# Kernel optimization log

Measured on AMD Instinct MI355X. Metric: run time of the kernel, lower is better.

The kernel has to match this reference:

```python
import jax, jax.numpy as jnp
import numpy as np

MAX_DISP = 4          # displacement radius -> 9x9 = 81 output channels
B, C, H, W = 8, 128, 96, 160


def setup_inputs() -> dict:
    key = jax.random.key(0)
    k1, k2 = jax.random.split(key)
    tensorFirst = jax.random.normal(k1, (B, C, H, W), dtype=jnp.float32)
    tensorSecond = jax.random.normal(k2, (B, C, H, W), dtype=jnp.float32)
    return {"tensorFirst": tensorFirst, "tensorSecond": tensorSecond}


def correlation(first, second):
    # first, second: [B, C, H, W]
    b, c, h, w = first.shape
    d = MAX_DISP
    pad = jnp.pad(second, ((0, 0), (0, 0), (d, d), (d, d)))  # [B,C,H+8,W+8]
    inv_c = jnp.asarray(1.0 / c, dtype=first.dtype)
    # channel order: (dy+4)*9 + (dx+4), dx fastest (matches CUDA kernel)
    chans = [
        (first * pad[:, :, dy:dy + h, dx:dx + w]).sum(axis=1) * inv_c
        for dy in range(2 * d + 1)
        for dx in range(2 * d + 1)
    ]
    return jnp.stack(chans, axis=1)  # [B, 81, H, W]


def reference(tensorFirst, tensorSecond):
    return correlation(tensorFirst, tensorSecond)
```

## Files before the change

kernel.cpp:

```cpp
#include <hip/hip_runtime.h>
#include <stdint.h>


typedef __attribute__((ext_vector_type(8))) short bf16x8;
typedef __attribute__((ext_vector_type(4))) float f32x4;

constexpr int Bn = 8, Cn = 128, Hn = 96, Wn = 160;
constexpr int CHS = Hn * Wn;

__device__ __forceinline__ uint32_t bf16rne(float f) {
    uint32_t u = __float_as_uint(f);
    return (u + 0x7FFFu + ((u >> 16) & 1u)) >> 16;
}
__device__ __forceinline__ uint32_t pk(float a, float b) {
    return bf16rne(a) | (bf16rne(b) << 16);
}

__global__ __launch_bounds__(512, 4)
void corrfused(const float* __restrict__ first, const float* __restrict__ second,
               float* __restrict__ out)
{
    __shared__ uint4 smem[16 * 32 * 4];

    const int tid  = threadIdx.x;
    const int w    = tid >> 6;
    const int lane = tid & 63;
    const int quad = lane >> 4;
    const int n16  = lane & 15;
    const int r    = w;

    const int d    = (int)blockIdx.x + 10 * ((int)blockIdx.y + 12 * (int)blockIdx.z);
    const int tile = (d & 7) * 120 + (d >> 3);
    const int b    = tile / 120;
    const int rem  = tile % 120;
    const int y0   = (rem / 10) * 8;
    const int x0   = (rem % 10) * 16;
    const int y    = y0 + r;

    const float* sb = second + (size_t)b * Cn * CHS;
    int goff[4], lpos[4];
    bool val[4];
    #pragma unroll
    for (int i = 0; i < 4; ++i) {
        int e   = tid + i * 512;
        int row = e >> 7;
        int xw  = (e >> 2) & 31;
        int q   = e & 3;
        int gy  = y0 + row - 4, gx = x0 + xw - 8;
        val[i]  = (gy >= 0) && (gy < Hn) && (gx >= 0) && (gx < Wn);
        goff[i] = val[i] ? (8 * q * CHS + gy * Wn + gx) : 0;
        lpos[i] = (row * 32 + xw) * 4 + ((q + xw + (xw >> 2)) & 3);
    }

    int bo[2];
    #pragma unroll
    for (int t = 0; t < 2; ++t) {
        int xwr = 16 * t + n16;
        bo[t] = xwr * 4 + ((quad + xwr + (xwr >> 2)) & 3);
    }

    const float* fp = first + (size_t)b * Cn * CHS + (size_t)y * Wn + x0 + n16;

    f32x4 acc[9][2];
    #pragma unroll
    for (int dy = 0; dy < 9; ++dy)
        #pragma unroll
        for (int t = 0; t < 2; ++t)
            acc[dy][t] = (f32x4){0.f, 0.f, 0.f, 0.f};

    float f0[2][8];
    #pragma unroll
    for (int i = 0; i < 2; ++i)
        #pragma unroll
        for (int j = 0; j < 8; ++j)
            f0[i][j] = sb[goff[i] + (size_t)j * CHS];

    #pragma unroll
    for (int kc = 0; kc < 4; ++kc) {
        #pragma unroll
        for (int i = 0; i < 2; ++i) {
            uint4 o;
            o.x = pk(f0[i][0], f0[i][1]); o.y = pk(f0[i][2], f0[i][3]);
            o.z = pk(f0[i][4], f0[i][5]); o.w = pk(f0[i][6], f0[i][7]);
            if (!val[i]) o = make_uint4(0u, 0u, 0u, 0u);
            smem[lpos[i]] = o;
        }
        float f1[2][8], fa[8];
        #pragma unroll
        for (int i = 0; i < 2; ++i)
            #pragma unroll
            for (int j = 0; j < 8; ++j)
                f1[i][j] = sb[goff[2 + i] + (size_t)(32 * kc + j) * CHS];
        #pragma unroll
        for (int j = 0; j < 8; ++j)
            fa[j] = fp[(size_t)(32 * kc + 8 * quad + j) * CHS];
        #pragma unroll
        for (int i = 0; i < 2; ++i) {
            uint4 o;
            o.x = pk(f1[i][0], f1[i][1]); o.y = pk(f1[i][2], f1[i][3]);
            o.z = pk(f1[i][4], f1[i][5]); o.w = pk(f1[i][6], f1[i][7]);
            if (!val[2 + i]) o = make_uint4(0u, 0u, 0u, 0u);
            smem[lpos[2 + i]] = o;
        }
        bf16x8 aF;
        {
            union { uint32_t u[4]; bf16x8 v; } cv;
            cv.u[0] = pk(fa[0], fa[1]); cv.u[1] = pk(fa[2], fa[3]);
            cv.u[2] = pk(fa[4], fa[5]); cv.u[3] = pk(fa[6], fa[7]);
            aF = cv.v;
        }
        __syncthreads();
        if (kc < 3) {
            #pragma unroll
            for (int i = 0; i < 2; ++i)
                #pragma unroll
                for (int j = 0; j < 8; ++j)
                    f0[i][j] = sb[goff[i] + (size_t)(32 * (kc + 1) + j) * CHS];
        }
        #pragma unroll
        for (int dy = 0; dy < 9; ++dy) {
            const int rb = (r + dy) * 128;
            #pragma unroll
            for (int t = 0; t < 2; ++t) {
                union { uint4 u; bf16x8 v; } bf;
                bf.u = smem[rb + bo[t]];
                acc[dy][t] = __builtin_amdgcn_mfma_f32_16x16x32_bf16(
                                 aF, bf.v, acc[dy][t], 0, 0, 0);
            }
        }
        __syncthreads();
    }

    const float inv = 1.0f / 128.0f;
    float* sm = (float*)smem;
    float* ob = out + (size_t)b * 81 * CHS + (size_t)y * Wn + x0;
    const int wb = w * 540;
    #pragma unroll
    for (int ck = 0; ck < 3; ++ck) {
        #pragma unroll
        for (int dd = 0; dd < 3; ++dd)
            #pragma unroll
            for (int t = 0; t < 2; ++t)
                #pragma unroll
                for (int reg = 0; reg < 4; ++reg) {
                    int mm  = quad * 4 + reg;
                    int dxc = 16 * t + n16 - mm - 4;
                    if (dxc >= 0 && dxc <= 8)
                        sm[wb + (dd * 9 + dxc) * 20 + mm] = acc[ck * 3 + dd][t][reg] * inv;
                }
        __syncthreads();
        #pragma unroll
        for (int ii = 0; ii < 2; ++ii) {
            int slot = lane + ii * 64;
            if (slot < 108) {
                int chn = slot >> 2, g = slot & 3;
                float4 v = *(const float4*)&sm[wb + chn * 20 + 4 * g];
                int ch = (ck * 3 + chn / 9) * 9 + chn % 9;
                *(float4*)(ob + (size_t)ch * CHS + 4 * g) = v;
            }
        }
        __syncthreads();
    }
}

extern "C" void kernel_launch(void* const* d_in, const int* in_sizes, int n_in,
                              void* d_out, int out_size, void* d_ws, size_t ws_size,
                              hipStream_t stream) {
    (void)in_sizes; (void)n_in; (void)d_ws; (void)ws_size; (void)out_size;
    const float* first  = (const float*)d_in[0];
    const float* second = (const float*)d_in[1];
    float* out = (float*)d_out;
    corrfused<<<dim3(Wn / 16, Hn / 8, Bn), dim3(512, 1, 1), 0, stream>>>(
        first, second, out);
}
```

Before: 182.2 us.

## Split into bf16 padded prepass and register-resident MFMA correlation kernel

Adds a prepass kernel that converts the second tensor into a zero-padded, channel-octet-packed bf16 layout in workspace. A new main kernel then loads those octets straight from global memory into registers without LDS staging or barriers. Each wave covers a 2x8 pixel patch across ten vertical offsets, and the kernel keeps the LDS transpose only for output stores. The aim is to remove repeated conversion and padding work and the shared-memory synchronisation in the main loop, at the cost of an extra launch and a workspace write and read. The old kernel is kept as a fallback when the workspace is too small.

```diff
diff --git a/kernel.cpp b/kernel.cpp
--- a/kernel.cpp
+++ b/kernel.cpp
@@ -7,6 +7,10 @@
 
 constexpr int Bn = 8, Cn = 128, Hn = 96, Wn = 160;
 constexpr int CHS = Hn * Wn;
+constexpr int YP  = Hn + 8;
+constexpr int XPD = Wn + 16;
+constexpr size_t SECP_OCTS  = (size_t)Bn * 16 * YP * XPD;
+constexpr size_t SECP_BYTES = SECP_OCTS * 16;
 
 __device__ __forceinline__ uint32_t bf16rne(float f) {
     uint32_t u = __float_as_uint(f);
@@ -16,9 +20,124 @@
     return bf16rne(a) | (bf16rne(b) << 16);
 }
 
+__global__ __launch_bounds__(256)
+void prepass(const float* __restrict__ sec, uint4* __restrict__ secp)
+{
+    const int idx = blockIdx.x * 256 + threadIdx.x;
+    const int xp  = idx % XPD;
+    const int t1  = idx / XPD;
+    const int yp  = t1 % YP;
+    const int t2  = t1 / YP;
+    const int oc  = t2 & 15;
+    const int b   = t2 >> 4;
+    const int y = yp - 4, x = xp - 8;
+    uint4 o = make_uint4(0u, 0u, 0u, 0u);
+    if (y >= 0 && y < Hn && x >= 0 && x < Wn) {
+        const float* src = sec + ((size_t)b * Cn + 8 * oc) * CHS + (size_t)y * Wn + x;
+        float f[8];
+        #pragma unroll
+        for (int j = 0; j < 8; ++j) f[j] = src[(size_t)j * CHS];
+        o.x = pk(f[0], f[1]); o.y = pk(f[2], f[3]);
+        o.z = pk(f[4], f[5]); o.w = pk(f[6], f[7]);
+    }
+    secp[idx] = o;
+}
+
+__global__ __launch_bounds__(256, 4)
+void corrmain(const float* __restrict__ first, const uint4* __restrict__ secp,
+              float* __restrict__ out)
+{
+    __shared__ float sm[4 * 1952];
+
+    const int tid  = threadIdx.x;
+    const int w    = tid >> 6;
+    const int lane = tid & 63;
+    const int quad = lane >> 4;
+    const int n16  = lane & 15;
+    const int s    = w & 1;
+    const int rp   = w >> 1;
+
+    const int d    = (int)blockIdx.x + 10 * ((int)blockIdx.y + 24 * (int)blockIdx.z);
+    const int tile = (d & 7) * 240 + (d >> 3);
+    const int b    = tile / 240;
+    const int rem  = tile % 240;
+    const int y0   = (rem / 10) * 4;
+    const int x0   = (rem % 10) * 16;
+
+    const uint4* sb = secp
+        + ((size_t)(b * 16 + quad) * YP + (y0 + 2 * rp)) * XPD
+        + x0 + 8 * s + 4 + n16;
+
+    uint4 cur[10];
+    #pragma unroll
+    for (int zi = 0; zi < 10; ++zi) cur[zi] = sb[(size_t)zi * XPD];
+
+    bf16x8 aF[4];
+    {
+        const float* fp = first + (size_t)b * Cn * CHS
+                        + (size_t)(y0 + 2 * rp + (n16 >> 3)) * Wn
+                        + x0 + 8 * s + (n16 & 7);
+        #pragma unroll
+        for (int kc = 0; kc < 4; ++kc) {
+            float f[8];
+            #pragma unroll
+            for (int j = 0; j < 8; ++j)
+                f[j] = fp[(size_t)(32 * kc + 8 * quad + j) * CHS];
+            union { uint32_t u[4]; bf16x8 v; } cv;
+            cv.u[0] = pk(f[0], f[1]); cv.u[1] = pk(f[2], f[3]);
+            cv.u[2] = pk(f[4], f[5]); cv.u[3] = pk(f[6], f[7]);
+            aF[kc] = cv.v;
+        }
+    }
+
+    f32x4 acc[10];
+    #pragma unroll
+    for (int zi = 0; zi < 10; ++zi) acc[zi] = (f32x4){0.f, 0.f, 0.f, 0.f};
+
+    #pragma unroll
+    for (int kc = 0; kc < 4; ++kc) {
+        #pragma unroll
+        for (int zi = 0; zi < 10; ++zi) {
+            union { uint4 u; bf16x8 v; } bf;
+            bf.u = cur[zi];
+            if (kc < 3)
+                cur[zi] = sb[(size_t)((kc + 1) * 4 * YP + zi) * XPD];
+            acc[zi] = __builtin_amdgcn_mfma_f32_16x16x32_bf16(
+                          aF[kc], bf.v, acc[zi], 0, 0, 0);
+        }
+    }
+
+    const float inv = 1.0f / 128.0f;
+    const int wb = w * 1952;
+    #pragma unroll
+    for (int zi = 0; zi < 10; ++zi)
+        #pragma unroll
+        for (int reg = 0; reg < 4; ++reg) {
+            const int rh  = quad >> 1;
+            const int px  = (quad & 1) * 4 + reg;
+            const int dyc = zi - rh;
+            const int dxc = n16 - px;
+            if (dyc >= 0 && dyc <= 8 && dxc >= 0 && dxc <= 8)
+                sm[wb + ((rh * 81) + dyc * 9 + dxc) * 12 + px] = acc[zi][reg] * inv;
+        }
+    __syncthreads();
+    float* ob = out + (size_t)b * 81 * CHS + (size_t)(y0 + 2 * rp) * Wn + x0 + 8 * s;
+    #pragma unroll
+    for (int ii = 0; ii < 6; ++ii) {
+        int slot = lane + ii * 64;
+        if (slot < 324) {
+            int rh  = (slot >= 162) ? 1 : 0;
+            int rm  = slot - 162 * rh;
+            int c   = rm >> 1, g = rm & 1;
+            float4 v = *(const float4*)&sm[wb + (rh * 81 + c) * 12 + 4 * g];
+            *(float4*)(ob + (size_t)c * CHS + (size_t)rh * Wn + 4 * g) = v;
+        }
+    }
+}
+
 __global__ __launch_bounds__(512, 4)
-void corrfused(const float* __restrict__ first, const float* __restrict__ second,
-               float* __restrict__ out)
+void corrfb(const float* __restrict__ first, const float* __restrict__ second,
+            float* __restrict__ out)
 {
     __shared__ uint4 smem[16 * 32 * 4];
 
@@ -166,10 +285,18 @@
 extern "C" void kernel_launch(void* const* d_in, const int* in_sizes, int n_in,
                               void* d_out, int out_size, void* d_ws, size_t ws_size,
                               hipStream_t stream) {
-    (void)in_sizes; (void)n_in; (void)d_ws; (void)ws_size; (void)out_size;
+    (void)in_sizes; (void)n_in; (void)out_size;
     const float* first  = (const float*)d_in[0];
     const float* second = (const float*)d_in[1];
     float* out = (float*)d_out;
-    corrfused<<<dim3(Wn / 16, Hn / 8, Bn), dim3(512, 1, 1), 0, stream>>>(
-        first, second, out);
-}
+
+    if (ws_size >= SECP_BYTES) {
+        uint4* secp = (uint4*)d_ws;
+        prepass<<<dim3((unsigned)(SECP_OCTS / 256), 1, 1), dim3(256, 1, 1), 0, stream>>>(
+            second, secp);
+        corrmain<<<dim3(10, 24, 8), dim3(256, 1, 1), 0, stream>>>(first, secp, out);
+    } else {
+        corrfb<<<dim3(Wn / 16, Hn / 8, Bn), dim3(512, 1, 1), 0, stream>>>(
+            first, second, out);
+    }
+}
```

New measurement: 190.7 us. +4.7%, slower.
